# Kernel tuning notes

Hardware: AMD Instinct MI355X
Metric: run time of the kernel (lower is better)

Reference implementation:

```python
import jax, jax.numpy as jnp
import numpy as np

FORGET_BIAS = 1.0  # tf LSTMCell default

def _lstm_step(c, h, xt, W, b):
    # tf LSTMCell: gates = [x, h] @ W + b, split order (i, j, f, o)
    gates = jnp.concatenate([xt, h], axis=-1) @ W + b
    i, j, f, o = jnp.split(gates, 4, axis=-1)
    c_new = c * jax.nn.sigmoid(f + FORGET_BIAS) + jax.nn.sigmoid(i) * jnp.tanh(j)
    h_new = jnp.tanh(c_new) * jax.nn.sigmoid(o)
    return c_new, h_new

def setup_inputs() -> dict:
    key = jax.random.key(0)
    k1, k2, k3 = jax.random.split(key, 3)
    B, T, H = 512, 1024, 64
    x = jax.random.normal(k1, (B, T, 1), dtype=jnp.float32)
    W1 = jax.random.normal(k2, (1 + H, 4 * H), dtype=jnp.float32) * 0.1
    b1 = jnp.zeros((4 * H,), dtype=jnp.float32)
    W2 = jax.random.normal(k3, (H + 1, 4 * 1), dtype=jnp.float32) * 0.1
    b2 = jnp.zeros((4,), dtype=jnp.float32)
    return {"x": x, "W1": W1, "b1": b1, "W2": W2, "b2": b2}

def reference(x, W1, b1, W2, b2):
    B, T, _ = x.shape
    H = W1.shape[1] // 4
    xs = jnp.swapaxes(x, 0, 1)  # [T, B, 1]

    def step(carry, xt):
        c1, h1, c2, h2 = carry
        c1, h1 = _lstm_step(c1, h1, xt, W1, b1)   # layer 1: in=1, hidden=64
        c2, h2 = _lstm_step(c2, h2, h1, W2, b2)   # layer 2: in=64, hidden=1
        return (c1, h1, c2, h2), h2

    init = (jnp.zeros((B, H), x.dtype), jnp.zeros((B, H), x.dtype),
            jnp.zeros((B, 1), x.dtype), jnp.zeros((B, 1), x.dtype))
    _, ys = jax.lax.scan(step, init, xs)  # ys: [T, B, 1]
    return jnp.swapaxes(ys, 0, 1)  # [B, T, 1]
```

## Files before the change

### kernel.cpp

```cpp
#include <hip/hip_runtime.h>


#define TT 1024

__device__ __forceinline__ float fsig(float x) {
    return __builtin_amdgcn_rcpf(1.f + __expf(-x));
}
__device__ __forceinline__ float ftanh(float x) {
    return 1.f - 2.f * __builtin_amdgcn_rcpf(1.f + __expf(2.f * x));
}

template <int Ctrl, int Rmask>
__device__ __forceinline__ float dpp_add(float x) {
    int t = __builtin_amdgcn_update_dpp(0, __float_as_int(x), Ctrl, Rmask, 0xf, true);
    return x + __int_as_float(t);
}
__device__ __forceinline__ float wave_sum64(float x) {
    x = dpp_add<0x111, 0xf>(x);
    x = dpp_add<0x112, 0xf>(x);
    x = dpp_add<0x114, 0xf>(x);
    x = dpp_add<0x118, 0xf>(x);
    x = dpp_add<0x142, 0xa>(x);
    x = dpp_add<0x143, 0xc>(x);
    return x;
}

__global__ __launch_bounds__(320, 3) void lstm2_kernel(
    const float* __restrict__ x,
    const float* __restrict__ W1,
    const float* __restrict__ b1,
    const float* __restrict__ W2,
    const float* __restrict__ b2,
    float* __restrict__ y)
{
    __shared__ __align__(16) float xs[TT];
    __shared__ __align__(16) float h1s[64];
    __shared__ __align__(16) float gs[2][4][64];
    __shared__ float dbuf[2][4];

    const int tid  = threadIdx.x;
    const int b    = blockIdx.x;
    const int lane = tid & 63;
    const int g    = tid >> 6;

    if (tid < 256) {
        const float4* xrow = (const float4*)(x + (size_t)b * TT);
        ((float4*)xs)[tid] = xrow[tid];
    }

    float w[65];
    float bias = 0.f, w2g = 0.f;
    if (g < 4) {
#pragma unroll
        for (int k = 0; k < 65; ++k) w[k] = W1[k * 256 + tid];
        bias = b1[tid];
        w2g  = W2[lane * 4 + g];
    }

    const float w2h0 = W2[256], w2h1 = W2[257], w2h2 = W2[258], w2h3 = W2[259];
    const float b20 = b2[0], b21 = b2[1], b22 = b2[2], b23 = b2[3];

    float c1 = 0.f;
    float c2 = 0.f, h2 = 0.f;

    if (tid < 64) h1s[tid] = 0.f;
    __syncthreads();

    float* yrow = y + (size_t)b * TT;

    for (int t = 0; t < TT; ++t) {
        const int par = t & 1;
        if (g < 4) {
            const float xt = xs[t];
            float a0 = fmaf(xt, w[0], bias), a1 = 0.f, a2 = 0.f, a3 = 0.f;
#pragma unroll
            for (int kk = 0; kk < 16; ++kk) {
                float4 h4 = ((const float4*)h1s)[kk];
                a0 = fmaf(h4.x, w[1 + 4*kk + 0], a0);
                a1 = fmaf(h4.y, w[1 + 4*kk + 1], a1);
                a2 = fmaf(h4.z, w[1 + 4*kk + 2], a2);
                a3 = fmaf(h4.w, w[1 + 4*kk + 3], a3);
            }
            float gate = (a0 + a1) + (a2 + a3);
            float act;
            if (g == 1)      act = ftanh(gate);
            else if (g == 2) act = fsig(gate + 1.f);
            else             act = fsig(gate);
            gs[par][g][lane] = act;
        }
        __syncthreads();
        if (g < 4) {
            const float i_ = gs[par][0][lane], j_ = gs[par][1][lane];
            const float f_ = gs[par][2][lane], o_ = gs[par][3][lane];
            c1 = fmaf(c1, f_, i_ * j_);
            const float h1 = ftanh(c1) * o_;
            h1s[lane] = h1;
            float p = wave_sum64(h1 * w2g);
            if (lane == 63) dbuf[par][g] = p;
        } else if (t > 0 && lane == 0) {
            const int pp = par ^ 1;
            const float d0 = dbuf[pp][0], d1 = dbuf[pp][1];
            const float d2 = dbuf[pp][2], d3 = dbuf[pp][3];
            const float i2 = fsig (fmaf(h2, w2h0, d0) + b20);
            const float j2 = ftanh(fmaf(h2, w2h1, d1) + b21);
            const float f2 = fsig (fmaf(h2, w2h2, d2) + b22 + 1.f);
            const float o2 = fsig (fmaf(h2, w2h3, d3) + b23);
            c2 = fmaf(c2, f2, i2 * j2);
            h2 = ftanh(c2) * o2;
            yrow[t - 1] = h2;
        }
    }
    __syncthreads();
    if (g == 4 && lane == 0) {
        const int pp = (TT - 1) & 1;
        const float d0 = dbuf[pp][0], d1 = dbuf[pp][1];
        const float d2 = dbuf[pp][2], d3 = dbuf[pp][3];
        const float i2 = fsig (fmaf(h2, w2h0, d0) + b20);
        const float j2 = ftanh(fmaf(h2, w2h1, d1) + b21);
        const float f2 = fsig (fmaf(h2, w2h2, d2) + b22 + 1.f);
        const float o2 = fsig (fmaf(h2, w2h3, d3) + b23);
        c2 = fmaf(c2, f2, i2 * j2);
        h2 = ftanh(c2) * o2;
        yrow[TT - 1] = h2;
    }
}

extern "C" void kernel_launch(void* const* d_in, const int* in_sizes, int n_in,
                              void* d_out, int out_size, void* d_ws, size_t ws_size,
                              hipStream_t stream) {
    const float* x  = (const float*)d_in[0];
    const float* W1 = (const float*)d_in[1];
    const float* b1 = (const float*)d_in[2];
    const float* W2 = (const float*)d_in[3];
    const float* b2 = (const float*)d_in[4];
    float* y = (float*)d_out;
    lstm2_kernel<<<512, 320, 0, stream>>>(x, W1, b1, W2, b2, y);
}
```

Measured before the change: 795.7 us.

## Split layer-1 gate dot product across two half-waves per column

The layer-1 recurrent matvec is split along the hidden dimension. Two half-waves each compute 32 of the 64 products for a gate column and combine them with a cross-half shuffle, so the block grows from 5 to 9 waves. The aim is to halve the serial FMA chain and the LDS reads per thread on the latency-bound recurrence. In exchange, each barrier now has more waves to synchronise and the extra waves redundantly compute the cell update.

```diff
diff --git a/kernel.cpp b/kernel.cpp
--- a/kernel.cpp
+++ b/kernel.cpp
@@ -25,7 +25,7 @@
     return x;
 }
 
-__global__ __launch_bounds__(320, 3) void lstm2_kernel(
+__global__ __launch_bounds__(576) void lstm2_kernel(
     const float* __restrict__ x,
     const float* __restrict__ W1,
     const float* __restrict__ b1,
@@ -41,21 +41,31 @@
     const int tid  = threadIdx.x;
     const int b    = blockIdx.x;
     const int lane = tid & 63;
-    const int g    = tid >> 6;
+    const int cw   = tid >> 6;
+    const int half = lane >> 5;
+    const int l31  = lane & 31;
+    const int col  = (cw << 5) | l31;
+    const int g    = cw >> 1;
 
     if (tid < 256) {
-        const float4* xrow = (const float4*)(x + (size_t)b * TT);
-        ((float4*)xs)[tid] = xrow[tid];
+        ((float4*)xs)[tid] = ((const float4*)(x + (size_t)b * TT))[tid];
     }
 
-    float w[65];
+    float w[33];
     float bias = 0.f, w2g = 0.f;
-    if (g < 4) {
+    if (cw < 8) {
+        if (half == 0) {
+            w[0] = W1[col];
+            bias = b1[col];
 #pragma unroll
-        for (int k = 0; k < 65; ++k) w[k] = W1[k * 256 + tid];
-        bias = b1[tid];
-        w2g  = W2[lane * 4 + g];
+            for (int j = 1; j <= 32; ++j) w[j] = W1[j * 256 + col];
+        } else {
+            w[0] = 0.f;
+#pragma unroll
+            for (int j = 1; j <= 32; ++j) w[j] = W1[(32 + j) * 256 + col];
+        }
     }
+    if (cw < 4) w2g = W2[lane * 4 + cw];
 
     const float w2h0 = W2[256], w2h1 = W2[257], w2h2 = W2[258], w2h3 = W2[259];
     const float b20 = b2[0], b21 = b2[1], b22 = b2[2], b23 = b2[3];
@@ -67,36 +77,40 @@
     __syncthreads();
 
     float* yrow = y + (size_t)b * TT;
+    const int hbase = half << 3;
 
     for (int t = 0; t < TT; ++t) {
         const int par = t & 1;
-        if (g < 4) {
+        if (cw < 8) {
             const float xt = xs[t];
             float a0 = fmaf(xt, w[0], bias), a1 = 0.f, a2 = 0.f, a3 = 0.f;
 #pragma unroll
-            for (int kk = 0; kk < 16; ++kk) {
-                float4 h4 = ((const float4*)h1s)[kk];
-                a0 = fmaf(h4.x, w[1 + 4*kk + 0], a0);
-                a1 = fmaf(h4.y, w[1 + 4*kk + 1], a1);
-                a2 = fmaf(h4.z, w[1 + 4*kk + 2], a2);
-                a3 = fmaf(h4.w, w[1 + 4*kk + 3], a3);
+            for (int q = 0; q < 8; ++q) {
+                float4 h4 = ((const float4*)h1s)[hbase + q];
+                a0 = fmaf(h4.x, w[1 + 4*q], a0);
+                a1 = fmaf(h4.y, w[2 + 4*q], a1);
+                a2 = fmaf(h4.z, w[3 + 4*q], a2);
+                a3 = fmaf(h4.w, w[4 + 4*q], a3);
             }
-            float gate = (a0 + a1) + (a2 + a3);
+            float p = (a0 + a1) + (a2 + a3);
+            p += __shfl_xor(p, 32);
             float act;
-            if (g == 1)      act = ftanh(gate);
-            else if (g == 2) act = fsig(gate + 1.f);
-            else             act = fsig(gate);
-            gs[par][g][lane] = act;
+            if (g == 1)      act = ftanh(p);
+            else if (g == 2) act = fsig(p + 1.f);
+            else             act = fsig(p);
+            if (half == 0) gs[par][g][(cw & 1) * 32 + l31] = act;
         }
         __syncthreads();
-        if (g < 4) {
+        if (cw < 8) {
             const float i_ = gs[par][0][lane], j_ = gs[par][1][lane];
             const float f_ = gs[par][2][lane], o_ = gs[par][3][lane];
             c1 = fmaf(c1, f_, i_ * j_);
             const float h1 = ftanh(c1) * o_;
             h1s[lane] = h1;
-            float p = wave_sum64(h1 * w2g);
-            if (lane == 63) dbuf[par][g] = p;
+            if (cw < 4) {
+                float p = wave_sum64(h1 * w2g);
+                if (lane == 63) dbuf[par][cw] = p;
+            }
         } else if (t > 0 && lane == 0) {
             const int pp = par ^ 1;
             const float d0 = dbuf[pp][0], d1 = dbuf[pp][1];
@@ -111,7 +125,7 @@
         }
     }
     __syncthreads();
-    if (g == 4 && lane == 0) {
+    if (cw == 8 && lane == 0) {
         const int pp = (TT - 1) & 1;
         const float d0 = dbuf[pp][0], d1 = dbuf[pp][1];
         const float d2 = dbuf[pp][2], d3 = dbuf[pp][3];
@@ -134,5 +148,5 @@
     const float* W2 = (const float*)d_in[3];
     const float* b2 = (const float*)d_in[4];
     float* y = (float*)d_out;
-    lstm2_kernel<<<512, 320, 0, stream>>>(x, W1, b1, W2, b2, y);
+    lstm2_kernel<<<512, 576, 0, stream>>>(x, W1, b1, W2, b2, y);
 }
```

After: 779.2 us. 1.02x faster.

## Split layer-1 gate dot products across quarter-waves with 1024-thread blocks

Applied to the files above, without the earlier changes.

Each layer-1 gate column's 64-term dot product over h1 is now split across four 16-lane quarter-waves and recombined with two xor shuffles. This cuts the serial FMA chain and the per-thread weight registers (17 instead of 65). The block grows to 16 waves, and every wave redundantly recomputes the cell state and h1. The aim is a shorter per-timestep critical path in this latency-bound recurrence. The cost is a 16-wave barrier each step, extra shuffles, and more waves competing per SIMD.

```diff
diff --git a/kernel.cpp b/kernel.cpp
--- a/kernel.cpp
+++ b/kernel.cpp
@@ -25,7 +25,7 @@
     return x;
 }
 
-__global__ __launch_bounds__(320, 3) void lstm2_kernel(
+__global__ __launch_bounds__(1024) void lstm2_kernel(
     const float* __restrict__ x,
     const float* __restrict__ W1,
     const float* __restrict__ b1,
@@ -41,21 +41,25 @@
     const int tid  = threadIdx.x;
     const int b    = blockIdx.x;
     const int lane = tid & 63;
-    const int g    = tid >> 6;
+    const int wv   = tid >> 6;
+    const int q    = lane >> 4;
+    const int l15  = lane & 15;
+    const int col  = (wv << 4) | l15;
+    const int g    = wv >> 2;
 
     if (tid < 256) {
-        const float4* xrow = (const float4*)(x + (size_t)b * TT);
-        ((float4*)xs)[tid] = xrow[tid];
+        ((float4*)xs)[tid] = ((const float4*)(x + (size_t)b * TT))[tid];
     }
 
-    float w[65];
-    float bias = 0.f, w2g = 0.f;
-    if (g < 4) {
+    float w[17];
+    float bias = 0.f;
+    if (q == 0) { w[0] = W1[col]; bias = b1[col]; }
+    else        { w[0] = 0.f; }
 #pragma unroll
-        for (int k = 0; k < 65; ++k) w[k] = W1[k * 256 + tid];
-        bias = b1[tid];
-        w2g  = W2[lane * 4 + g];
-    }
+    for (int j = 1; j <= 16; ++j) w[j] = W1[(16 * q + j) * 256 + col];
+
+    float w2g = 0.f;
+    if (wv < 4) w2g = W2[lane * 4 + wv];
 
     const float w2h0 = W2[256], w2h1 = W2[257], w2h2 = W2[258], w2h3 = W2[259];
     const float b20 = b2[0], b21 = b2[1], b22 = b2[2], b23 = b2[3];
@@ -67,37 +71,40 @@
     __syncthreads();
 
     float* yrow = y + (size_t)b * TT;
+    const int hbase = q << 2;
 
     for (int t = 0; t < TT; ++t) {
         const int par = t & 1;
-        if (g < 4) {
-            const float xt = xs[t];
-            float a0 = fmaf(xt, w[0], bias), a1 = 0.f, a2 = 0.f, a3 = 0.f;
+        const float xt = xs[t];
+        float a0 = fmaf(xt, w[0], bias), a1 = 0.f, a2 = 0.f, a3 = 0.f;
 #pragma unroll
-            for (int kk = 0; kk < 16; ++kk) {
-                float4 h4 = ((const float4*)h1s)[kk];
-                a0 = fmaf(h4.x, w[1 + 4*kk + 0], a0);
-                a1 = fmaf(h4.y, w[1 + 4*kk + 1], a1);
-                a2 = fmaf(h4.z, w[1 + 4*kk + 2], a2);
-                a3 = fmaf(h4.w, w[1 + 4*kk + 3], a3);
-            }
-            float gate = (a0 + a1) + (a2 + a3);
-            float act;
-            if (g == 1)      act = ftanh(gate);
-            else if (g == 2) act = fsig(gate + 1.f);
-            else             act = fsig(gate);
-            gs[par][g][lane] = act;
+        for (int jj = 0; jj < 4; ++jj) {
+            float4 h4 = ((const float4*)h1s)[hbase + jj];
+            a0 = fmaf(h4.x, w[1 + 4*jj], a0);
+            a1 = fmaf(h4.y, w[2 + 4*jj], a1);
+            a2 = fmaf(h4.z, w[3 + 4*jj], a2);
+            a3 = fmaf(h4.w, w[4 + 4*jj], a3);
         }
+        float p = (a0 + a1) + (a2 + a3);
+        p += __shfl_xor(p, 16);
+        p += __shfl_xor(p, 32);
+        float act;
+        if (g == 1)      act = ftanh(p);
+        else if (g == 2) act = fsig(p + 1.f);
+        else             act = fsig(p);
+        if (q == 0) gs[par][g][((wv & 3) << 4) | l15] = act;
+
         __syncthreads();
-        if (g < 4) {
-            const float i_ = gs[par][0][lane], j_ = gs[par][1][lane];
-            const float f_ = gs[par][2][lane], o_ = gs[par][3][lane];
-            c1 = fmaf(c1, f_, i_ * j_);
-            const float h1 = ftanh(c1) * o_;
-            h1s[lane] = h1;
-            float p = wave_sum64(h1 * w2g);
-            if (lane == 63) dbuf[par][g] = p;
-        } else if (t > 0 && lane == 0) {
+
+        const float i_ = gs[par][0][lane], j_ = gs[par][1][lane];
+        const float f_ = gs[par][2][lane], o_ = gs[par][3][lane];
+        c1 = fmaf(c1, f_, i_ * j_);
+        const float h1 = ftanh(c1) * o_;
+        h1s[lane] = h1;
+        if (wv < 4) {
+            float pd = wave_sum64(h1 * w2g);
+            if (lane == 63) dbuf[par][wv] = pd;
+        } else if (wv == 15 && t > 0 && lane == 0) {
             const int pp = par ^ 1;
             const float d0 = dbuf[pp][0], d1 = dbuf[pp][1];
             const float d2 = dbuf[pp][2], d3 = dbuf[pp][3];
@@ -111,7 +118,7 @@
         }
     }
     __syncthreads();
-    if (g == 4 && lane == 0) {
+    if (wv == 15 && lane == 0) {
         const int pp = (TT - 1) & 1;
         const float d0 = dbuf[pp][0], d1 = dbuf[pp][1];
         const float d2 = dbuf[pp][2], d3 = dbuf[pp][3];
@@ -134,5 +141,5 @@
     const float* W2 = (const float*)d_in[3];
     const float* b2 = (const float*)d_in[4];
     float* y = (float*)d_out;
-    lstm2_kernel<<<512, 320, 0, stream>>>(x, W1, b1, W2, b2, y);
+    lstm2_kernel<<<512, 1024, 0, stream>>>(x, W1, b1, W2, b2, y);
 }
```

New measurement: 1.048 ms. +31.7%, slower.
